# Kernel optimization log

Hardware: AMD Instinct MI355X
Metric: run time of the kernel (lower is better)

Reference implementation:

```python
import jax, jax.numpy as jnp
import numpy as np

H, C = 5, 128          # heads, hidden_channels
NUM_GRAPHS = 500
N_NODES, N_EDGES = 20000, 320000


def gat_layer(x, edge_attr, src, dst, W, We, a_src, a_dst, a_edge, b):
    """PyG GATConv with edge_dim, add_self_loops=True, fill_value='mean', concat heads."""
    N = x.shape[0]
    ed = edge_attr.dtype
    # self-loop edge_attr = scatter-mean of incoming edge_attr per target node
    deg = jax.ops.segment_sum(jnp.ones((dst.shape[0],), ed), dst, num_segments=N)
    loop_attr = jax.ops.segment_sum(edge_attr, dst, num_segments=N) / jnp.maximum(deg, 1.0)[:, None]
    loop = jnp.arange(N, dtype=src.dtype)
    s = jnp.concatenate([src, loop])
    d = jnp.concatenate([dst, loop])
    ea = jnp.concatenate([edge_attr, loop_attr], axis=0)
    h = (x @ W).reshape(N, H, C)            # [N,H,C]
    e = (ea @ We).reshape(-1, H, C)         # [E2,H,C]
    a_l = (h * a_src).sum(-1)               # [N,H]
    a_r = (h * a_dst).sum(-1)               # [N,H]
    a_e = (e * a_edge).sum(-1)              # [E2,H]
    alpha = jax.nn.leaky_relu(a_l[s] + a_r[d] + a_e, 0.2)
    # segment softmax over destination neighborhoods
    amax = jax.ops.segment_max(alpha, d, num_segments=N)
    ex = jnp.exp(alpha - amax[d])
    denom = jax.ops.segment_sum(ex, d, num_segments=N)
    att = ex / (denom[d] + 1e-16)           # [E2,H]
    msg = h[s] * att[..., None]             # [E2,H,C]
    out = jax.ops.segment_sum(msg, d, num_segments=N).reshape(N, H * C)
    return out + b


def setup_inputs() -> dict:
    key = jax.random.key(0)
    ks = jax.random.split(key, 24)
    p = lambda k, sh: (jax.random.normal(k, sh, dtype=jnp.float32) * 0.05)
    inp = {
        "x": jax.random.normal(ks[0], (N_NODES, 43), dtype=jnp.float32),
        "edge_attr": jax.random.normal(ks[1], (N_EDGES, 10), dtype=jnp.float32),
        "W1": p(ks[2], (43, H * C)),   "We1": p(ks[3], (10, H * C)),
        "asrc1": p(ks[4], (H, C)), "adst1": p(ks[5], (H, C)), "aedge1": p(ks[6], (H, C)),
        "b1": jnp.zeros((H * C,), jnp.float32),
        "W2": p(ks[7], (H * C, H * C)), "We2": p(ks[8], (10, H * C)),
        "asrc2": p(ks[9], (H, C)), "adst2": p(ks[10], (H, C)), "aedge2": p(ks[11], (H, C)),
        "b2": jnp.zeros((H * C,), jnp.float32),
        "W3": p(ks[12], (H * C, H * C)), "We3": p(ks[13], (10, H * C)),
        "asrc3": p(ks[14], (H, C)), "adst3": p(ks[15], (H, C)), "aedge3": p(ks[16], (H, C)),
        "b3": jnp.zeros((H * C,), jnp.float32),
        "Wlin": p(ks[17], (H * C, 1)), "blin": jnp.zeros((1,), jnp.float32),
        "edge_index": jax.random.randint(ks[18], (2, N_EDGES), 0, N_NODES, dtype=jnp.int32),
        "batch": jnp.sort(jax.random.randint(ks[19], (N_NODES,), 0, NUM_GRAPHS, dtype=jnp.int32)),
    }
    return inp


def reference(x, edge_attr, W1, We1, asrc1, adst1, aedge1, b1,
              W2, We2, asrc2, adst2, aedge2, b2,
              W3, We3, asrc3, adst3, aedge3, b3,
              Wlin, blin, edge_index, batch):
    src, dst = edge_index[0], edge_index[1]
    h = jax.nn.relu(gat_layer(x, edge_attr, src, dst, W1, We1, asrc1, adst1, aedge1, b1))
    h = jax.nn.relu(gat_layer(h, edge_attr, src, dst, W2, We2, asrc2, adst2, aedge2, b2))
    h = gat_layer(h, edge_attr, src, dst, W3, We3, asrc3, adst3, aedge3, b3)
    # global mean pool over graphs
    cnt = jax.ops.segment_sum(jnp.ones((h.shape[0],), h.dtype), batch, num_segments=NUM_GRAPHS)
    pooled = jax.ops.segment_sum(h, batch, num_segments=NUM_GRAPHS) / jnp.maximum(cnt, 1.0)[:, None]
    return (pooled @ Wlin + blin).squeeze(-1)   # [NUM_GRAPHS]
```

## Files before the change

### kernel.cpp

```cpp
#include <hip/hip_runtime.h>

#define N_NODESC 20000
#define N_EDGESC 320000
#define HC 640
#define NGRAPH 500

typedef unsigned short u16;
typedef unsigned int u32;
typedef __attribute__((ext_vector_type(8))) short bf16x8;
typedef __attribute__((ext_vector_type(4))) float f32x4;

__device__ __forceinline__ float wred_sum(float v){
  #pragma unroll
  for(int o=32;o;o>>=1) v += __shfl_xor(v,o,64);
  return v;
}
__device__ __forceinline__ float lrelu(float x){ return x>0.f? x:0.2f*x; }

__device__ __forceinline__ u16 f2bf(float f){
  u32 u=__float_as_uint(f);
  u32 r=u+0x7FFFu+((u>>16)&1u);
  return (u16)(r>>16);
}
__device__ __forceinline__ float bf2f(u16 s){ return __uint_as_float(((u32)s)<<16); }
__device__ __forceinline__ float bflo(u32 w){ return __uint_as_float(w<<16); }
__device__ __forceinline__ float bfhi(u32 w){ return __uint_as_float(w&0xFFFF0000u); }

__device__ __forceinline__ void gload16(const void* g, void* l){
  __builtin_amdgcn_global_load_lds((const __attribute__((address_space(1))) void*)g,
                                   (__attribute__((address_space(3))) void*)l, 16, 0, 0);
}

__device__ __forceinline__ size_t fidx(int r, int k, int KB){
  return ((size_t)(r>>4)*KB + (k>>5))*512 + (((k>>3)&3)*16 + (r&15))*8 + (k&7);
}


__global__ void k_count(const int* __restrict__ dst, int* __restrict__ cnt){
  int i=blockIdx.x*blockDim.x+threadIdx.x;
  if(i>=N_EDGESC) return;
  atomicAdd(&cnt[dst[i]],1);
}

__global__ void k_scan(const int* __restrict__ cnt, int* __restrict__ rptr, int* __restrict__ pos){
  __shared__ int ps[1024];
  int t=threadIdx.x;
  const int CH=20;
  int beg=t*CH, end=min(beg+CH, N_NODESC);
  int s=0;
  for(int i=beg;i<end;i++) s+=cnt[i];
  ps[t]=s; __syncthreads();
  for(int off=1;off<1024;off<<=1){
    int v=(t>=off)? ps[t-off]:0;
    __syncthreads();
    ps[t]+=v;
    __syncthreads();
  }
  int base=ps[t]-s;
  for(int i=beg;i<end;i++){ rptr[i]=base; pos[i]=base; base+=cnt[i]; }
}

__global__ void k_scatter(const int* __restrict__ dst, const int* __restrict__ src,
                          const float* __restrict__ eattr, int* __restrict__ pos,
                          int* __restrict__ srcE, int* __restrict__ dstC,
                          float* __restrict__ eattrC){
  int i=blockIdx.x*blockDim.x+threadIdx.x;
  if(i>=N_EDGESC) return;
  int d=dst[i];
  int j=atomicAdd(&pos[d],1);
  dstC[j]=d;
  srcE[j]=src[i];
  const float* ep=&eattr[(size_t)i*10];
  float* op=&eattrC[(size_t)j*10];
  #pragma unroll
  for(int k=0;k<10;k++) op[k]=ep[k];
}

__global__ __launch_bounds__(256) void k_loop_attr(const float* __restrict__ eattrC,
    const int* __restrict__ rptr, const int* __restrict__ cnt,
    float* __restrict__ lattr){
  int tid=threadIdx.x, lane=tid&63;
  int n=blockIdx.x*4+(tid>>6);
  if(n>=N_NODESC) return;
  int beg=rptr[n], deg=cnt[n];
  float s[10]={0,0,0,0,0,0,0,0,0,0};
  for(int off=lane; off<deg; off+=64){
    const float* ep=&eattrC[(size_t)(beg+off)*10];
    #pragma unroll
    for(int k=0;k<10;k++) s[k]+=ep[k];
  }
  float inv=1.f/fmaxf((float)deg,1.f);
  #pragma unroll
  for(int k=0;k<10;k++){
    float tot=wred_sum(s[k]);
    if(lane==0) lattr[(size_t)n*10+k]=tot*inv;
  }
}


__global__ void k_padx(const float* __restrict__ x, float* __restrict__ xp){
  int idx=blockIdx.x*blockDim.x+threadIdx.x;
  if(idx>=N_NODESC*64) return;
  int n=idx>>6, kk=idx&63;
  xp[idx] = kk<43 ? x[n*43+kk] : 0.f;
}

__global__ void k_conv_w3(const float* __restrict__ W0, const float* __restrict__ W1,
                          const float* __restrict__ W2,
                          u16* __restrict__ hi, u16* __restrict__ lo){
  const int R0=HC*64, R1=R0+HC*HC;
  const int TOT=R1+HC*HC;
  int idx=blockIdx.x*blockDim.x+threadIdx.x;
  if(idx>=TOT) return;
  const float* W; int local, KP, KL, base;
  if(idx<R0){ W=W0; local=idx; KP=64; KL=43; base=0; }
  else if(idx<R1){ W=W1; local=idx-R0; KP=HC; KL=HC; base=R0; }
  else { W=W2; local=idx-R1; KP=HC; KL=HC; base=R1; }
  int n=local/KP, kk=local-n*KP;
  float v = kk<KL ? W[(size_t)kk*HC+n] : 0.f;
  u16 h=f2bf(v);
  size_t off=(size_t)base + fidx(n,kk,KP>>5);
  hi[off]=h;
  lo[off]=f2bf(v-bf2f(h));
}


__global__ void k_ve3(const float* __restrict__ We0, const float* __restrict__ ae0,
                      const float* __restrict__ We1, const float* __restrict__ ae1,
                      const float* __restrict__ We2, const float* __restrict__ ae2,
                      float* __restrict__ ve3){
  int t=threadIdx.x;
  if(t>=150) return;
  int L=t/50, r=t-50*L, k=r/5, h=r%5;
  const float* We = (L==0)?We0:(L==1)?We1:We2;
  const float* ae = (L==0)?ae0:(L==1)?ae1:ae2;
  float s=0.f;
  for(int c=0;c<128;c++) s += We[k*HC + h*128 + c]*ae[h*128+c];
  ve3[t]=s;
}

__global__ void k_vs0(const float* __restrict__ W0, const float* __restrict__ asrc,
                      const float* __restrict__ adst,
                      float* __restrict__ VS, float* __restrict__ VD){
  int t=threadIdx.x;
  if(t>=320) return;
  int k=t/5, h=t%5;
  float sv=0.f, dv=0.f;
  if(k<43){
    for(int c=0;c<128;c++){
      float wv=W0[(size_t)k*HC + h*128 + c];
      sv+=wv*asrc[h*128+c];
      dv+=wv*adst[h*128+c];
    }
  }
  VS[t]=sv; VD[t]=dv;
}

__global__ __launch_bounds__(256) void k_alar0(const float* __restrict__ x,
    const float* __restrict__ VS, const float* __restrict__ VD,
    float* __restrict__ al, float* __restrict__ ar){
  __shared__ float vs[320], vd[320];
  if(threadIdx.x<320){ vs[threadIdx.x]=VS[threadIdx.x]; vd[threadIdx.x]=VD[threadIdx.x]; }
  __syncthreads();
  int idx=blockIdx.x*blockDim.x+threadIdx.x;
  if(idx>=N_NODESC*5) return;
  int n=idx/5, h=idx-5*n;
  float sa=0.f, sd=0.f;
  const float* xr=&x[(size_t)n*43];
  for(int k=0;k<43;k++){
    float xv=xr[k];
    sa+=xv*vs[k*5+h];
    sd+=xv*vd[k*5+h];
  }
  al[idx]=sa; ar[idx]=sd;
}

__global__ void k_cb(const float* __restrict__ bias, const float* __restrict__ wlin,
                     float* __restrict__ cb){
  int lane=threadIdx.x;
  float s=0.f;
  for(int c=lane;c<HC;c+=64) s+=bias[c]*wlin[c];
  s=wred_sum(s);
  if(lane==0) cb[0]=s;
}

__global__ __launch_bounds__(256) void k_edge_terms3(const float* __restrict__ eattrC,
    const float* __restrict__ lattr, const float* __restrict__ ve3,
    float* __restrict__ aeC3, float* __restrict__ ael3){
  __shared__ float ves[150];
  if(threadIdx.x<150) ves[threadIdx.x]=ve3[threadIdx.x];
  __syncthreads();
  const int NEDGET=N_EDGESC+N_NODESC*5;
  int idx=blockIdx.x*blockDim.x+threadIdx.x;
  if(idx>=3*NEDGET) return;
  int L=idx/NEDGET, r=idx-L*NEDGET;
  const float* vl=&ves[L*50];
  if(r<N_EDGESC){
    float ev[10];
    const float* ep=&eattrC[(size_t)r*10];
    #pragma unroll
    for(int k=0;k<10;k++) ev[k]=ep[k];
    #pragma unroll
    for(int hh=0;hh<5;hh++){
      float s=0.f;
      #pragma unroll
      for(int k=0;k<10;k++) s+=ev[k]*vl[k*5+hh];
      aeC3[(size_t)L*N_EDGESC*5 + (size_t)r*5+hh]=s;
    }
  }else{
    int t=r-N_EDGESC;
    int n=t/5, h=t-5*n;
    float s=0.f;
    #pragma unroll
    for(int k=0;k<10;k++) s+=lattr[(size_t)n*10+k]*vl[k*5+h];
    ael3[(size_t)L*N_NODESC*5 + t]=s;
  }
}

__global__ void k_edgew(const int* __restrict__ srcE, const int* __restrict__ dstC,
                        const float* __restrict__ al, const float* __restrict__ ar,
                        const float* __restrict__ aeC, float* __restrict__ wE){
  int j=blockIdx.x*blockDim.x+threadIdx.x;
  if(j>=N_EDGESC) return;
  int s=srcE[j], d=dstC[j];
  const float* av=&aeC[(size_t)j*5];
  float* wp=&wE[(size_t)j*5];
  #pragma unroll
  for(int h=0;h<5;h++)
    wp[h]=__expf(lrelu(al[s*5+h]+ar[d*5+h]+av[h]));
}


__global__ __launch_bounds__(256) void k_aggx(const float* __restrict__ xp,
    const int* __restrict__ srcE, const int* __restrict__ rptr, const int* __restrict__ cnt,
    const float* __restrict__ al, const float* __restrict__ ar, const float* __restrict__ ael,
    const float* __restrict__ wE,
    u16* __restrict__ aggx, float* __restrict__ den0){
  const size_t HSZ=(size_t)N_NODESC*64;
  int tid=threadIdx.x, lane=tid&63;
  int n=blockIdx.x*4+(tid>>6);
  if(n>=N_NODESC) return;
  float den[5], acc[5];
  #pragma unroll
  for(int h=0;h<5;h++)
    den[h]=__expf(lrelu(al[n*5+h]+ar[n*5+h]+ael[n*5+h]));
  float xn=xp[(size_t)n*64+lane];
  #pragma unroll
  for(int h=0;h<5;h++) acc[h]=den[h]*xn;
  int beg=rptr[n], end=beg+cnt[n];
  int j=beg;
  for(; j+7<end; j+=8){
    int sj[8]; float xv[8];
    #pragma unroll
    for(int u=0;u<8;u++) sj[u]=srcE[j+u];
    #pragma unroll
    for(int u=0;u<8;u++) xv[u]=xp[(size_t)sj[u]*64+lane];
    #pragma unroll
    for(int u=0;u<8;u++){
      const float* wp=&wE[(size_t)(j+u)*5];
      #pragma unroll
      for(int h=0;h<5;h++){
        float w=wp[h];
        den[h]+=w;
        acc[h]+=w*xv[u];
      }
    }
  }
  for(; j<end; j++){
    int sj=srcE[j];
    float xv=xp[(size_t)sj*64+lane];
    const float* wp=&wE[(size_t)j*5];
    #pragma unroll
    for(int h=0;h<5;h++){
      float w=wp[h];
      den[h]+=w;
      acc[h]+=w*xv;
    }
  }
  size_t fo=fidx(n,lane,2);
  #pragma unroll
  for(int h=0;h<5;h++) aggx[(size_t)h*HSZ+fo]=f2bf(acc[h]);
  if(lane<5) den0[(size_t)n*5+lane]=den[lane];
}

__global__ __launch_bounds__(256,3) void k_gemm_l0b(
    const u16* __restrict__ AGX,
    const u16* __restrict__ Bhi, const u16* __restrict__ Blo,
    const float* __restrict__ den0, const float* __restrict__ bias,
    u16* __restrict__ A1, int M, int nblk){
  const size_t HSZ=(size_t)N_NODESC*64;
  __shared__ u16 lds[2*3*4096];
  int tid=threadIdx.x;
  int lane=tid&63;
  int w=tid>>6;
  int l15=lane&15, lg=lane>>4;
  int orig=blockIdx.x;
  int q=nblk>>3, r=nblk&7;
  int xcd=orig&7, off=orig>>3;
  int wg=(xcd<r? xcd*(q+1) : r*(q+1)+(xcd-r)*q)+off;
  int by=wg/5, bx=wg-5*by;
  int row0=by*128, col0=bx*128;
  int wr=w>>1, wc=w&1;
  const u16* A=AGX+(size_t)bx*HSZ;

  f32x4 zero = {0.f,0.f,0.f,0.f};
  f32x4 acc[4][4];
  #pragma unroll
  for(int i=0;i<4;i++)
    #pragma unroll
    for(int j=0;j<4;j++) acc[i][j]=zero;

  auto stage=[&](int b, int k0){
    u16* base = lds + b*3*4096;
    int kb=k0>>5;
    #pragma unroll
    for(int c=0;c<2;c++){
      int sb=w+4*c;
      size_t af=((size_t)((row0>>4)+sb)*2 + kb)*512 + lane*8;
      size_t bf=((size_t)((col0>>4)+sb)*2 + kb)*512 + lane*8;
      gload16(A+af, base + sb*512);
      gload16(Bhi+bf, base+4096 + sb*512);
      gload16(Blo+bf, base+8192 + sb*512);
    }
  };

  stage(0,0);
  __syncthreads();
  int cur=0;
  for(int t=0;t<2;t++){
    if(t==0) stage(1,32);
    u16* cb = lds + cur*3*4096;
    bf16x8 ah[4], bh[4], bl[4];
    #pragma unroll
    for(int i=0;i<4;i++){
      ah[i]=*(const bf16x8*)&cb[(wr*4+i)*512 + lane*8];
      bh[i]=*(const bf16x8*)&cb[4096+(wc*4+i)*512 + lane*8];
      bl[i]=*(const bf16x8*)&cb[8192+(wc*4+i)*512 + lane*8];
    }
    #pragma unroll
    for(int i=0;i<4;i++)
      #pragma unroll
      for(int j=0;j<4;j++){
        acc[i][j]=__builtin_amdgcn_mfma_f32_16x16x32_bf16(ah[i],bh[j],acc[i][j],0,0,0);
        acc[i][j]=__builtin_amdgcn_mfma_f32_16x16x32_bf16(ah[i],bl[j],acc[i][j],0,0,0);
      }
    __syncthreads();
    cur^=1;
  }

  #pragma unroll
  for(int i=0;i<4;i++){
    #pragma unroll
    for(int j=0;j<4;j++){
      int col=col0+wc*64+j*16+l15;
      float bv=bias[col];
      #pragma unroll
      for(int rr=0;rr<4;rr++){
        int row=row0+wr*64+i*16+lg*4+rr;
        if(row<M){
          float dv=den0[(size_t)row*5+bx];
          float v=acc[i][j][rr]/(dv+1e-16f)+bv;
          v=fmaxf(v,0.f);
          A1[fidx(row,col,20)]=f2bf(v);
        }
      }
    }
  }
}


template<bool HB, bool QOUT>
__global__ __launch_bounds__(256,4) void k_gemm64(
    const u16* __restrict__ A,
    const u16* __restrict__ B,
    const float* __restrict__ asrc, const float* __restrict__ adst,
    const float* __restrict__ wlin,
    u16* __restrict__ hb, float* __restrict__ al, float* __restrict__ ar,
    float* __restrict__ qn,
    int M, int KP, int nblk){
  __shared__ u16 lds[3*6144];
  int tid=threadIdx.x;
  int lane=tid&63;
  int w=tid>>6;
  int l15=lane&15, lg=lane>>4;
  int orig=blockIdx.x;
  int q=nblk>>3, r=nblk&7;
  int xcd=orig&7, off=orig>>3;
  int wg=(xcd<r? xcd*(q+1) : r*(q+1)+(xcd-r)*q)+off;
  int by=wg/5, bx=wg-5*by;
  int row0=by*64, col0=bx*128;
  int KB=KP>>5;

  f32x4 zero = {0.f,0.f,0.f,0.f};
  f32x4 acc[4][2];
  #pragma unroll
  for(int i=0;i<4;i++){ acc[i][0]=zero; acc[i][1]=zero; }

  auto stage=[&](int b, int k0){
    u16* base = lds + b*6144;
    int kb=k0>>5;
    size_t af=((size_t)((row0>>4)+w)*KB + kb)*512 + lane*8;
    gload16(A+af, base + w*512);
    #pragma unroll
    for(int c=0;c<2;c++){
      int sb=w+4*c;
      size_t bf=((size_t)((col0>>4)+sb)*KB + kb)*512 + lane*8;
      gload16(B+bf, base+2048 + sb*512);
    }
  };

  int nt=KP/32;
  stage(0,0);
  if(nt>1) stage(1,32);
  for(int t=0;t<nt;t++){
    int nb=t+2;
    if(nb<nt) stage(nb%3, nb*32);
    if(nb<nt)      { asm volatile("s_waitcnt vmcnt(6)" ::: "memory"); }
    else if(t+1<nt){ asm volatile("s_waitcnt vmcnt(3)" ::: "memory"); }
    else           { asm volatile("s_waitcnt vmcnt(0)" ::: "memory"); }
    __builtin_amdgcn_sched_barrier(0);
    __builtin_amdgcn_s_barrier();
    u16* cb = lds + (t%3)*6144;
    bf16x8 ah[4], bh[2];
    #pragma unroll
    for(int i=0;i<4;i++) ah[i]=*(const bf16x8*)&cb[i*512 + lane*8];
    #pragma unroll
    for(int j=0;j<2;j++) bh[j]=*(const bf16x8*)&cb[2048+(w*2+j)*512 + lane*8];
    #pragma unroll
    for(int i=0;i<4;i++){
      acc[i][0]=__builtin_amdgcn_mfma_f32_16x16x32_bf16(ah[i],bh[0],acc[i][0],0,0,0);
      acc[i][1]=__builtin_amdgcn_mfma_f32_16x16x32_bf16(ah[i],bh[1],acc[i][1],0,0,0);
    }
    __builtin_amdgcn_s_barrier();
  }
  __syncthreads();

  float asv[2], adv[2], wlv[2];
  #pragma unroll
  for(int j=0;j<2;j++){
    int c=col0+w*32+j*16+l15;
    asv[j]=asrc[c]; adv[j]=adst[c];
    if(QOUT) wlv[j]=wlin[c];
  }
  if(HB){
    #pragma unroll
    for(int i=0;i<4;i++){
      #pragma unroll
      for(int j=0;j<2;j++){
        #pragma unroll
        for(int rr=0;rr<4;rr++){
          int row=row0+i*16+lg*4+rr;
          if(row<M)
            hb[(size_t)row*HC + ((w&1)*32+j*16+l15)*10 + bx*2+(w>>1)]=f2bf(acc[i][j][rr]);
        }
      }
    }
  }
  float* redAl=(float*)lds;
  float* redAr=redAl+256;
  float* redQ =redAr+256;
  #pragma unroll
  for(int i=0;i<4;i++){
    #pragma unroll
    for(int rr=0;rr<4;rr++){
      float sa=0.f, sd=0.f, sq=0.f;
      #pragma unroll
      for(int j=0;j<2;j++){
        sa+=acc[i][j][rr]*asv[j];
        sd+=acc[i][j][rr]*adv[j];
        if(QOUT) sq+=acc[i][j][rr]*wlv[j];
      }
      #pragma unroll
      for(int o=1;o<16;o<<=1){
        sa+=__shfl_xor(sa,o,64); sd+=__shfl_xor(sd,o,64);
        if(QOUT) sq+=__shfl_xor(sq,o,64);
      }
      if(l15==0){
        int lr=i*16+lg*4+rr;
        redAl[lr*4+w]=sa; redAr[lr*4+w]=sd;
        if(QOUT) redQ[lr*4+w]=sq;
      }
    }
  }
  __syncthreads();
  if(tid<64){
    int row=row0+tid;
    if(row<M){
      al[(size_t)row*5+bx]=redAl[tid*4]+redAl[tid*4+1]+redAl[tid*4+2]+redAl[tid*4+3];
      ar[(size_t)row*5+bx]=redAr[tid*4]+redAr[tid*4+1]+redAr[tid*4+2]+redAr[tid*4+3];
      if(QOUT) qn[(size_t)row*5+bx]=redQ[tid*4]+redQ[tid*4+1]+redQ[tid*4+2]+redQ[tid*4+3];
    }
  }
}

__global__ __launch_bounds__(256) void k_agg(const u16* __restrict__ hb, const int* __restrict__ srcE,
    const int* __restrict__ rptr, const int* __restrict__ cnt,
    const float* __restrict__ al, const float* __restrict__ ar, const float* __restrict__ ael,
    const float* __restrict__ wE, const float* __restrict__ bias,
    u16* __restrict__ ohi){
  int tid=threadIdx.x, lane=tid&63;
  int n=blockIdx.x*4+(tid>>6);
  if(n>=N_NODESC) return;
  float den[5], acc[10];
  #pragma unroll
  for(int h=0;h<5;h++)
    den[h]=__expf(lrelu(al[n*5+h]+ar[n*5+h]+ael[n*5+h]));
  {
    const u32* sp=(const u32*)(hb+(size_t)n*HC+lane*10);
    #pragma unroll
    for(int j2=0;j2<5;j2++){
      u32 wv=sp[j2];
      acc[2*j2]  =den[j2]*bflo(wv);
      acc[2*j2+1]=den[j2]*bfhi(wv);
    }
  }
  int beg=rptr[n], end=beg+cnt[n];
  int j=beg;
  for(; j+3<end; j+=4){
    int sj[4];
    #pragma unroll
    for(int u=0;u<4;u++) sj[u]=srcE[j+u];
    float w[4][5];
    #pragma unroll
    for(int u=0;u<4;u++){
      const float* wp=&wE[(size_t)(j+u)*5];
      #pragma unroll
      for(int h=0;h<5;h++) w[u][h]=wp[h];
    }
    u32 wv[4][5];
    #pragma unroll
    for(int u=0;u<4;u++){
      const u32* hr=(const u32*)(hb+(size_t)sj[u]*HC+lane*10);
      #pragma unroll
      for(int j2=0;j2<5;j2++) wv[u][j2]=hr[j2];
    }
    #pragma unroll
    for(int u=0;u<4;u++){
      #pragma unroll
      for(int j2=0;j2<5;j2++){
        den[j2]+=w[u][j2];
        acc[2*j2]  +=w[u][j2]*bflo(wv[u][j2]);
        acc[2*j2+1]+=w[u][j2]*bfhi(wv[u][j2]);
      }
    }
  }
  for(; j<end; j++){
    int sj=srcE[j];
    const float* wp=&wE[(size_t)j*5];
    float w[5];
    #pragma unroll
    for(int h=0;h<5;h++){ w[h]=wp[h]; den[h]+=w[h]; }
    const u32* hr=(const u32*)(hb+(size_t)sj*HC+lane*10);
    #pragma unroll
    for(int j2=0;j2<5;j2++){
      u32 wv=hr[j2];
      acc[2*j2]  +=w[j2]*bflo(wv);
      acc[2*j2+1]+=w[j2]*bfhi(wv);
    }
  }
  #pragma unroll
  for(int k=0;k<10;k++){
    int ccol=lane+64*k;
    float vv=acc[k]/(den[k>>1]+1e-16f)+bias[ccol];
    vv=fmaxf(vv,0.f);
    ohi[fidx(n,ccol,20)]=f2bf(vv);
  }
}

__global__ __launch_bounds__(256) void k_agg_last(const float* __restrict__ qn,
    const int* __restrict__ srcE, const int* __restrict__ rptr, const int* __restrict__ cnt,
    const float* __restrict__ al, const float* __restrict__ ar, const float* __restrict__ ael,
    const float* __restrict__ aeC, const float* __restrict__ cb,
    float* __restrict__ pnode){
  int tid=threadIdx.x;
  int sub=tid&15;
  int n=blockIdx.x*16+(tid>>4);
  if(n>=N_NODESC) return;
  float arn[5], den[5], qs[5];
  #pragma unroll
  for(int h=0;h<5;h++) arn[h]=ar[n*5+h];
  #pragma unroll
  for(int h=0;h<5;h++){ den[h]=0.f; qs[h]=0.f; }
  if(sub==0){
    #pragma unroll
    for(int h=0;h<5;h++){
      float pp=__expf(lrelu(al[n*5+h]+arn[h]+ael[n*5+h]));
      den[h]=pp; qs[h]=pp*qn[(size_t)n*5+h];
    }
  }
  int beg=rptr[n], deg=cnt[n];
  for(int off=sub; off<deg; off+=16){
    int j=beg+off;
    int s=srcE[j];
    const float* av=&aeC[(size_t)j*5];
    const float* qv=&qn[(size_t)s*5];
    #pragma unroll
    for(int h=0;h<5;h++){
      float pp=__expf(lrelu(al[s*5+h]+arn[h]+av[h]));
      den[h]+=pp; qs[h]+=pp*qv[h];
    }
  }
  #pragma unroll
  for(int h=0;h<5;h++){
    #pragma unroll
    for(int o=1;o<16;o<<=1){
      den[h]+=__shfl_xor(den[h],o,16);
      qs[h]+=__shfl_xor(qs[h],o,16);
    }
  }
  if(sub==0){
    float s=0.f;
    #pragma unroll
    for(int h=0;h<5;h++) s+=qs[h]/(den[h]+1e-16f);
    pnode[n]=s+cb[0];
  }
}

__global__ __launch_bounds__(256) void k_graphout(const float* __restrict__ pnode,
    const int* __restrict__ batch, const float* __restrict__ blin,
    float* __restrict__ out){
  int tid=threadIdx.x, lane=tid&63;
  int g=blockIdx.x*4+(tid>>6);
  if(g>=NGRAPH) return;
  auto lb=[&](int val){
    int lo=0, hi=N_NODESC;
    while(lo<hi){ int mid=(lo+hi)>>1; if(batch[mid]<val) lo=mid+1; else hi=mid; }
    return lo;
  };
  int s0=lb(g), s1=lb(g+1);
  float s=0.f;
  for(int i=s0+lane;i<s1;i+=64) s+=pnode[i];
  s=wred_sum(s);
  if(lane==0) out[g]=s/fmaxf((float)(s1-s0),1.f)+blin[0];
}


extern "C" void kernel_launch(void* const* d_in, const int* in_sizes, int n_in,
                              void* d_out, int out_size, void* d_ws, size_t ws_size,
                              hipStream_t stream){
  const float* x     = (const float*)d_in[0];
  const float* eattr = (const float*)d_in[1];
  const float* W[3]    ={(const float*)d_in[2],(const float*)d_in[8],(const float*)d_in[14]};
  const float* We[3]   ={(const float*)d_in[3],(const float*)d_in[9],(const float*)d_in[15]};
  const float* asrc[3] ={(const float*)d_in[4],(const float*)d_in[10],(const float*)d_in[16]};
  const float* adst[3] ={(const float*)d_in[5],(const float*)d_in[11],(const float*)d_in[17]};
  const float* aedge[3]={(const float*)d_in[6],(const float*)d_in[12],(const float*)d_in[18]};
  const float* bias[3] ={(const float*)d_in[7],(const float*)d_in[13],(const float*)d_in[19]};
  const float* Wlin  = (const float*)d_in[20];
  const float* blin  = (const float*)d_in[21];
  const int* eind    = (const int*)d_in[22];
  const int* srcp    = eind;
  const int* dstp    = eind + N_EDGESC;
  const int* batch   = (const int*)d_in[23];
  float* out = (float*)d_out;

  char* ws=(char*)d_ws;
  size_t o=0;
  auto alloc=[&](size_t bytes)->void*{ void* p=ws+o; o=(o+bytes+255)&~(size_t)255; return p; };
  u16* hb   =(u16*)alloc((size_t)N_NODESC*HC*2);
  u16* Ahi =(u16*)alloc((size_t)N_NODESC*HC*2);
  float* xp =(float*)alloc((size_t)N_NODESC*64*4);
  u16* aggx=(u16*)alloc((size_t)5*N_NODESC*64*2);
  const int WB0=0, WB1=HC*64, WB2=WB1+HC*HC;
  u16* Bthi3=(u16*)alloc((size_t)(WB2+HC*HC)*2);
  u16* Btlo3=(u16*)alloc((size_t)(WB2+HC*HC)*2);
  float* al   =(float*)alloc((size_t)N_NODESC*5*4);
  float* ar   =(float*)alloc((size_t)N_NODESC*5*4);
  float* qn   =(float*)alloc((size_t)N_NODESC*5*4);
  float* den0 =(float*)alloc((size_t)N_NODESC*5*4);
  float* ael3 =(float*)alloc((size_t)3*N_NODESC*5*4);
  float* aeC3 =(float*)alloc((size_t)3*N_EDGESC*5*4);
  float* wE   =(float*)alloc((size_t)N_EDGESC*5*4);
  float* lattr=(float*)alloc((size_t)N_NODESC*10*4);
  float* eattrC=(float*)alloc((size_t)N_EDGESC*10*4);
  float* ve3  =(float*)alloc(256*4);
  float* VS0  =(float*)alloc(320*4);
  float* VD0  =(float*)alloc(320*4);
  float* cbv  =(float*)alloc(64*4);
  float* pnode=(float*)alloc((size_t)N_NODESC*4);
  int* cntI   =(int*)alloc((size_t)N_NODESC*4);
  int* rptr   =(int*)alloc((size_t)N_NODESC*4);
  int* pos    =(int*)alloc((size_t)N_NODESC*4);
  int* srcE   =(int*)alloc((size_t)N_EDGESC*4);
  int* dstC   =(int*)alloc((size_t)N_EDGESC*4);

  hipMemsetAsync(cntI,0,(size_t)N_NODESC*4,stream);

  k_count<<<(N_EDGESC+255)/256,256,0,stream>>>(dstp,cntI);
  k_scan<<<1,1024,0,stream>>>(cntI,rptr,pos);
  k_scatter<<<(N_EDGESC+255)/256,256,0,stream>>>(dstp,srcp,eattr,pos,srcE,dstC,eattrC);
  k_loop_attr<<<(N_NODESC+3)/4,256,0,stream>>>(eattrC,rptr,cntI,lattr);
  k_padx<<<(N_NODESC*64+255)/256,256,0,stream>>>(x,xp);
  k_ve3<<<1,256,0,stream>>>(We[0],aedge[0],We[1],aedge[1],We[2],aedge[2],ve3);
  k_vs0<<<1,320,0,stream>>>(W[0],asrc[0],adst[0],VS0,VD0);
  k_cb<<<1,64,0,stream>>>(bias[2],Wlin,cbv);
  {
    int tot=WB2+HC*HC;
    k_conv_w3<<<(tot+255)/256,256,0,stream>>>(W[0],W[1],W[2],Bthi3,Btlo3);
  }
  {
    const int NEDGET=N_EDGESC+N_NODESC*5;
    k_edge_terms3<<<(3*NEDGET+255)/256,256,0,stream>>>(eattrC,lattr,ve3,aeC3,ael3);
  }
  k_alar0<<<(N_NODESC*5+255)/256,256,0,stream>>>(x,VS0,VD0,al,ar);

  const int NBLK0=5*((N_NODESC+127)/128);
  const int NBLK64=5*((N_NODESC+63)/64);

  k_edgew<<<(N_EDGESC+255)/256,256,0,stream>>>(srcE,dstC,al,ar,aeC3,wE);
  k_aggx<<<(N_NODESC+3)/4,256,0,stream>>>(xp,srcE,rptr,cntI,al,ar,ael3,wE,aggx,den0);
  k_gemm_l0b<<<NBLK0,256,0,stream>>>(aggx,Bthi3+WB0,Btlo3+WB0,den0,bias[0],Ahi,N_NODESC,NBLK0);

  {
    const float* aeL = aeC3 + (size_t)1*N_EDGESC*5;
    const float* aelL= ael3 + (size_t)1*N_NODESC*5;
    k_gemm64<true,false><<<NBLK64,256,0,stream>>>(Ahi,Bthi3+WB1,
        asrc[1],adst[1],Wlin,hb,al,ar,qn,N_NODESC,HC,NBLK64);
    k_edgew<<<(N_EDGESC+255)/256,256,0,stream>>>(srcE,dstC,al,ar,aeL,wE);
    k_agg<<<(N_NODESC+3)/4,256,0,stream>>>(hb,srcE,rptr,cntI,al,ar,aelL,wE,bias[1],Ahi);
  }
  {
    const float* aelL= ael3 + (size_t)2*N_NODESC*5;
    k_gemm64<false,true><<<NBLK64,256,0,stream>>>(Ahi,Bthi3+WB2,
        asrc[2],adst[2],Wlin,hb,al,ar,qn,N_NODESC,HC,NBLK64);
    k_agg_last<<<(N_NODESC+15)/16,256,0,stream>>>(qn,srcE,rptr,cntI,al,ar,aelL,aeC3+(size_t)2*N_EDGESC*5,cbv,pnode);
  }
  k_graphout<<<(NGRAPH+3)/4,256,0,stream>>>(pnode,batch,blin,out);
}
```

Baseline: 382.6 us.

## Store padded x as bf16, merge tiny setup kernels, 4-stage GEMM pipeline

The padded layer-0 input is now stored in bf16 instead of fp32, which halves the bytes gathered per edge in the first aggregation at some precision cost. The bias-Wlin dot product kernel is folded into the k_vs0 launch to save one kernel launch. k_gemm64 moves from a 3-buffer to a 4-buffer LDS ring and drops the trailing barrier per K step, with launch bounds lowered from 4 to 3 blocks per SM to fit the extra shared memory, which may reduce occupancy.

Result: no change. 379.2 us (-0.9%).

```diff
diff --git a/kernel.cpp b/kernel.cpp
--- a/kernel.cpp
+++ b/kernel.cpp
@@ -98,11 +98,12 @@
 }
 
 
-__global__ void k_padx(const float* __restrict__ x, float* __restrict__ xp){
+__global__ void k_padxb(const float* __restrict__ x, u16* __restrict__ xb){
   int idx=blockIdx.x*blockDim.x+threadIdx.x;
   if(idx>=N_NODESC*64) return;
   int n=idx>>6, kk=idx&63;
-  xp[idx] = kk<43 ? x[n*43+kk] : 0.f;
+  float v = kk<43 ? x[n*43+kk] : 0.f;
+  xb[idx]=f2bf(v);
 }
 
 __global__ void k_conv_w3(const float* __restrict__ W0, const float* __restrict__ W1,
@@ -141,19 +142,28 @@
 
 __global__ void k_vs0(const float* __restrict__ W0, const float* __restrict__ asrc,
                       const float* __restrict__ adst,
-                      float* __restrict__ VS, float* __restrict__ VD){
+                      const float* __restrict__ bias2, const float* __restrict__ wlin,
+                      float* __restrict__ VS, float* __restrict__ VD,
+                      float* __restrict__ cb){
   int t=threadIdx.x;
-  if(t>=320) return;
-  int k=t/5, h=t%5;
-  float sv=0.f, dv=0.f;
-  if(k<43){
-    for(int c=0;c<128;c++){
-      float wv=W0[(size_t)k*HC + h*128 + c];
-      sv+=wv*asrc[h*128+c];
-      dv+=wv*adst[h*128+c];
-    }
-  }
-  VS[t]=sv; VD[t]=dv;
+  if(t<320){
+    int k=t/5, h=t%5;
+    float sv=0.f, dv=0.f;
+    if(k<43){
+      for(int c=0;c<128;c++){
+        float wv=W0[(size_t)k*HC + h*128 + c];
+        sv+=wv*asrc[h*128+c];
+        dv+=wv*adst[h*128+c];
+      }
+    }
+    VS[t]=sv; VD[t]=dv;
+  }else{
+    int lane=t-320;
+    float s=0.f;
+    for(int c=lane;c<HC;c+=64) s+=bias2[c]*wlin[c];
+    s=wred_sum(s);
+    if(lane==0) cb[0]=s;
+  }
 }
 
 __global__ __launch_bounds__(256) void k_alar0(const float* __restrict__ x,
@@ -175,15 +185,6 @@
   al[idx]=sa; ar[idx]=sd;
 }
 
-__global__ void k_cb(const float* __restrict__ bias, const float* __restrict__ wlin,
-                     float* __restrict__ cb){
-  int lane=threadIdx.x;
-  float s=0.f;
-  for(int c=lane;c<HC;c+=64) s+=bias[c]*wlin[c];
-  s=wred_sum(s);
-  if(lane==0) cb[0]=s;
-}
-
 __global__ __launch_bounds__(256) void k_edge_terms3(const float* __restrict__ eattrC,
     const float* __restrict__ lattr, const float* __restrict__ ve3,
     float* __restrict__ aeC3, float* __restrict__ ael3){
@@ -231,7 +232,7 @@
 }
 
 
-__global__ __launch_bounds__(256) void k_aggx(const float* __restrict__ xp,
+__global__ __launch_bounds__(256) void k_aggx(const u16* __restrict__ xb,
     const int* __restrict__ srcE, const int* __restrict__ rptr, const int* __restrict__ cnt,
     const float* __restrict__ al, const float* __restrict__ ar, const float* __restrict__ ael,
     const float* __restrict__ wE,
@@ -244,7 +245,7 @@
   #pragma unroll
   for(int h=0;h<5;h++)
     den[h]=__expf(lrelu(al[n*5+h]+ar[n*5+h]+ael[n*5+h]));
-  float xn=xp[(size_t)n*64+lane];
+  float xn=bf2f(xb[(size_t)n*64+lane]);
   #pragma unroll
   for(int h=0;h<5;h++) acc[h]=den[h]*xn;
   int beg=rptr[n], end=beg+cnt[n];
@@ -254,7 +255,7 @@
     #pragma unroll
     for(int u=0;u<8;u++) sj[u]=srcE[j+u];
     #pragma unroll
-    for(int u=0;u<8;u++) xv[u]=xp[(size_t)sj[u]*64+lane];
+    for(int u=0;u<8;u++) xv[u]=bf2f(xb[(size_t)sj[u]*64+lane]);
     #pragma unroll
     for(int u=0;u<8;u++){
       const float* wp=&wE[(size_t)(j+u)*5];
@@ -268,7 +269,7 @@
   }
   for(; j<end; j++){
     int sj=srcE[j];
-    float xv=xp[(size_t)sj*64+lane];
+    float xv=bf2f(xb[(size_t)sj*64+lane]);
     const float* wp=&wE[(size_t)j*5];
     #pragma unroll
     for(int h=0;h<5;h++){
@@ -370,7 +371,7 @@
 
 
 template<bool HB, bool QOUT>
-__global__ __launch_bounds__(256,4) void k_gemm64(
+__global__ __launch_bounds__(256,3) void k_gemm64(
     const u16* __restrict__ A,
     const u16* __restrict__ B,
     const float* __restrict__ asrc, const float* __restrict__ adst,
@@ -378,7 +379,7 @@
     u16* __restrict__ hb, float* __restrict__ al, float* __restrict__ ar,
     float* __restrict__ qn,
     int M, int KP, int nblk){
-  __shared__ u16 lds[3*6144];
+  __shared__ u16 lds[4*6144];
   int tid=threadIdx.x;
   int lane=tid&63;
   int w=tid>>6;
@@ -411,16 +412,16 @@
 
   int nt=KP/32;
   stage(0,0);
-  if(nt>1) stage(1,32);
+  stage(1,32);
   for(int t=0;t<nt;t++){
     int nb=t+2;
-    if(nb<nt) stage(nb%3, nb*32);
+    if(nb<nt) stage(nb&3, nb*32);
     if(nb<nt)      { asm volatile("s_waitcnt vmcnt(6)" ::: "memory"); }
     else if(t+1<nt){ asm volatile("s_waitcnt vmcnt(3)" ::: "memory"); }
     else           { asm volatile("s_waitcnt vmcnt(0)" ::: "memory"); }
     __builtin_amdgcn_sched_barrier(0);
     __builtin_amdgcn_s_barrier();
-    u16* cb = lds + (t%3)*6144;
+    u16* cb = lds + (t&3)*6144;
     bf16x8 ah[4], bh[2];
     #pragma unroll
     for(int i=0;i<4;i++) ah[i]=*(const bf16x8*)&cb[i*512 + lane*8];
@@ -431,7 +432,6 @@
       acc[i][0]=__builtin_amdgcn_mfma_f32_16x16x32_bf16(ah[i],bh[0],acc[i][0],0,0,0);
       acc[i][1]=__builtin_amdgcn_mfma_f32_16x16x32_bf16(ah[i],bh[1],acc[i][1],0,0,0);
     }
-    __builtin_amdgcn_s_barrier();
   }
   __syncthreads();
 
@@ -659,7 +659,7 @@
   auto alloc=[&](size_t bytes)->void*{ void* p=ws+o; o=(o+bytes+255)&~(size_t)255; return p; };
   u16* hb   =(u16*)alloc((size_t)N_NODESC*HC*2);
   u16* Ahi =(u16*)alloc((size_t)N_NODESC*HC*2);
-  float* xp =(float*)alloc((size_t)N_NODESC*64*4);
+  u16* xb  =(u16*)alloc((size_t)N_NODESC*64*2);
   u16* aggx=(u16*)alloc((size_t)5*N_NODESC*64*2);
   const int WB0=0, WB1=HC*64, WB2=WB1+HC*HC;
   u16* Bthi3=(u16*)alloc((size_t)(WB2+HC*HC)*2);
@@ -690,10 +690,9 @@
   k_scan<<<1,1024,0,stream>>>(cntI,rptr,pos);
   k_scatter<<<(N_EDGESC+255)/256,256,0,stream>>>(dstp,srcp,eattr,pos,srcE,dstC,eattrC);
   k_loop_attr<<<(N_NODESC+3)/4,256,0,stream>>>(eattrC,rptr,cntI,lattr);
-  k_padx<<<(N_NODESC*64+255)/256,256,0,stream>>>(x,xp);
+  k_padxb<<<(N_NODESC*64+255)/256,256,0,stream>>>(x,xb);
   k_ve3<<<1,256,0,stream>>>(We[0],aedge[0],We[1],aedge[1],We[2],aedge[2],ve3);
-  k_vs0<<<1,320,0,stream>>>(W[0],asrc[0],adst[0],VS0,VD0);
-  k_cb<<<1,64,0,stream>>>(bias[2],Wlin,cbv);
+  k_vs0<<<1,384,0,stream>>>(W[0],asrc[0],adst[0],bias[2],Wlin,VS0,VD0,cbv);
   {
     int tot=WB2+HC*HC;
     k_conv_w3<<<(tot+255)/256,256,0,stream>>>(W[0],W[1],W[2],Bthi3,Btlo3);
@@ -708,7 +707,7 @@
   const int NBLK64=5*((N_NODESC+63)/64);
 
   k_edgew<<<(N_EDGESC+255)/256,256,0,stream>>>(srcE,dstC,al,ar,aeC3,wE);
-  k_aggx<<<(N_NODESC+3)/4,256,0,stream>>>(xp,srcE,rptr,cntI,al,ar,ael3,wE,aggx,den0);
+  k_aggx<<<(N_NODESC+3)/4,256,0,stream>>>(xb,srcE,rptr,cntI,al,ar,ael3,wE,aggx,den0);
   k_gemm_l0b<<<NBLK0,256,0,stream>>>(aggx,Bthi3+WB0,Btlo3+WB0,den0,bias[0],Ahi,N_NODESC,NBLK0);
 
   {
```
